# Performance work log

Measured on AMD Instinct MI355X. Metric: run time of the kernel, lower is better.

## Reference

```python
import math
import jax, jax.numpy as jnp
import numpy as np

B, T, D, NH = 4, 2048, 1024, 16
HS = D // NH
N_BUCKETS = 32
MAX_DIST = 128


def _relative_position_bucket(rp):
    # bidirectional T5 bucketing, n_buckets=32, max_distance=128
    nb = N_BUCKETS // 2  # 16
    buckets = (rp > 0).astype(jnp.int32) * nb
    rp = jnp.abs(rp)
    max_exact = nb // 2  # 8
    is_small = rp < max_exact
    me = max_exact - 1   # 7
    nbm = nb - 1         # 15
    rp_safe = jnp.maximum(rp, 1).astype(jnp.float32)
    rp_large = me + (jnp.log(rp_safe / me) / math.log(MAX_DIST / me) * (nbm - me)).astype(jnp.int32)
    rp_large = jnp.minimum(rp_large, nbm)
    buckets = buckets + jnp.where(is_small, rp, rp_large)
    return buckets


def compute_bias(rel_emb, qT, kT):
    ctx = jnp.arange(qT, dtype=jnp.int32)[:, None]
    mem = jnp.arange(kT, dtype=jnp.int32)[None, :]
    bucket = _relative_position_bucket(mem - ctx)  # [qT, kT]
    values = rel_emb[bucket]                        # [qT, kT, NH]
    return jnp.transpose(values, (2, 0, 1))[None]   # [1, NH, qT, kT]


def setup_inputs() -> dict:
    key = jax.random.key(0)
    ks = jax.random.split(key, 6)
    s = 0.02
    return {
        "queries": jax.random.normal(ks[0], (B, T, D), jnp.float32),
        "Wq": jax.random.normal(ks[1], (D, D), jnp.float32) * s,
        "Wk": jax.random.normal(ks[2], (D, D), jnp.float32) * s,
        "Wv": jax.random.normal(ks[3], (D, D), jnp.float32) * s,
        "Wo": jax.random.normal(ks[4], (D, D), jnp.float32) * s,
        "rel_emb": jax.random.normal(ks[5], (N_BUCKETS, NH), jnp.float32) * s,
    }


def reference(queries, Wq, Wk, Wv, Wo, rel_emb):
    b, t, d = queries.shape
    def split_heads(x):
        return jnp.transpose(x.reshape(b, t, NH, HS), (0, 2, 1, 3))  # [B, nh, T, hs]
    q = split_heads(queries @ Wq.T)
    k = split_heads(queries @ Wk.T)
    v = split_heads(queries @ Wv.T)
    att = jnp.einsum('bhqd,bhkd->bhqk', q, k) * (1.0 / math.sqrt(HS))
    att = att + compute_bias(rel_emb, t, t)
    att = jax.nn.softmax(att, axis=-1)
    o = jnp.einsum('bhqk,bhkd->bhqd', att, v)
    o = jnp.transpose(o, (0, 2, 1, 3)).reshape(b, t, d)
    return o @ Wo.T
```

## Files before the change

kernel.cpp:

```cpp
#include <hip/hip_runtime.h>
#include <math.h>

#define T_SEQ 2048
#define D_MODEL 1024
#define NHEADS 16
#define HSZ 64
#define BATCH 4

typedef __bf16 bf16x8 __attribute__((ext_vector_type(8)));
typedef __bf16 bf16x4 __attribute__((ext_vector_type(4)));
typedef short short4v __attribute__((ext_vector_type(4)));
typedef float f32x4 __attribute__((ext_vector_type(4)));
typedef float f32x16 __attribute__((ext_vector_type(16)));

__device__ __forceinline__ unsigned short f2bf(float f) {
    unsigned int u = __builtin_bit_cast(unsigned int, f);
    u += 0x7fff + ((u >> 16) & 1);
    return (unsigned short)(u >> 16);
}

__device__ __forceinline__ unsigned int pk2bf(float a, float b) {
#if __has_builtin(__builtin_amdgcn_cvt_pk_bf16_f32)
    typedef __bf16 bf16x2_t __attribute__((ext_vector_type(2)));
    bf16x2_t v = __builtin_amdgcn_cvt_pk_bf16_f32(a, b);
    return __builtin_bit_cast(unsigned int, v);
#else
    return (unsigned int)f2bf(a) | ((unsigned int)f2bf(b) << 16);
#endif
}

__device__ __forceinline__ float fexp2(float x) {
#if __has_builtin(__builtin_amdgcn_exp2f)
    return __builtin_amdgcn_exp2f(x);
#else
    return __builtin_exp2f(x);
#endif
}

__device__ __forceinline__ void gld_lds16(const void* g, void* lds) {
    __builtin_amdgcn_global_load_lds(
        (const __attribute__((address_space(1))) unsigned int*)g,
        (__attribute__((address_space(3))) unsigned int*)lds, 16, 0, 0);
}

__device__ __forceinline__ bf16x8 ld8(const unsigned short* p) {
    return *(const bf16x8*)p;
}

__device__ __forceinline__ float t5_bias(int delta, int h, const float* __restrict__ rel) {
    int bucket = delta > 0 ? 16 : 0;
    int arp = delta < 0 ? -delta : delta;
    if (arp < 8) {
        bucket += arp;
    } else {
        float f = logf((float)arp / 7.0f) * (8.0f / logf(128.0f / 7.0f));
        int rl = 7 + (int)f;
        bucket += rl < 15 ? rl : 15;
    }
    return rel[bucket * NHEADS + h] * 1.4426950408889634f;
}

__global__ void prep(const float* __restrict__ x,
                     const float* __restrict__ w0, const float* __restrict__ w1,
                     const float* __restrict__ w2, const float* __restrict__ w3,
                     unsigned short* __restrict__ Xbf,
                     unsigned short* __restrict__ Wbf) {
    int bid = blockIdx.x;
    int tid = threadIdx.x;
    if (bid < 8192) {
        int i = bid * 256 + tid;
        float4 v = ((const float4*)x)[i];
        ushort4 o;
        o.x = f2bf(v.x); o.y = f2bf(v.y); o.z = f2bf(v.z); o.w = f2bf(v.w);
        ((ushort4*)Xbf)[i] = o;
    } else {
        int wsel = (bid - 8192) >> 10;
        const float* srcs[4] = {w0, w1, w2, w3};
        int i = ((bid - 8192) & 1023) * 256 + tid;
        float4 v = ((const float4*)srcs[wsel])[i];
        ushort4 o;
        o.x = f2bf(v.x); o.y = f2bf(v.y); o.z = f2bf(v.z); o.w = f2bf(v.w);
        ((ushort4*)(Wbf + (size_t)wsel * 1048576))[i] = o;
    }
}

template<int MODE>
__global__ __launch_bounds__(256, 3) void gemm_bt(
    const unsigned short* __restrict__ A,
    const unsigned short* __restrict__ Bw,
    void* __restrict__ out)
{
    constexpr int K = 1024;
    __shared__ __align__(16) char smem[36864];
    unsigned short* As = (unsigned short*)smem;
    unsigned short* Bs = (unsigned short*)(smem + 16384);

    const int tid  = threadIdx.x;
    const int wave = tid >> 6;
    const int lane = tid & 63;
    const int quad = lane >> 4;
    const int l16  = lane & 15;
    const int wm   = wave >> 1;
    const int wn   = wave & 1;
    const int bn   = blockIdx.x;
    const int bm   = blockIdx.y;

    const int r_in = lane >> 3;
    const int lc   = (lane & 7) ^ r_in;

    f32x4 acc[4][4];
    #pragma unroll
    for (int m = 0; m < 4; ++m)
        #pragma unroll
        for (int n = 0; n < 4; ++n)
            acc[m][n] = f32x4{0.f, 0.f, 0.f, 0.f};

    const long a_row0 = (long)bm * 128;
    const long b_row0 = (long)bn * 128;

    for (int kt = 0; kt < K / 64; ++kt) {
        __syncthreads();
        const int k0 = kt * 64 + lc * 8;
        #pragma unroll
        for (int c = 0; c < 4; ++c) {
            int cc = wave * 4 + c;
            int r  = cc * 8 + r_in;
            gld_lds16(A  + (a_row0 + r) * K + k0, &As[cc * 512]);
            gld_lds16(Bw + (b_row0 + r) * K + k0, &Bs[cc * 512]);
        }
        __syncthreads();

        bf16x8 af[4][2], bf[4][2];
        #pragma unroll
        for (int m = 0; m < 4; ++m)
            #pragma unroll
            for (int ks = 0; ks < 2; ++ks) {
                int r  = wm * 64 + m * 16 + l16;
                int pc = (ks * 4 + quad) ^ (r & 7);
                af[m][ks] = ld8(&As[r * 64 + pc * 8]);
            }
        #pragma unroll
        for (int n = 0; n < 4; ++n)
            #pragma unroll
            for (int ks = 0; ks < 2; ++ks) {
                int r  = wn * 64 + n * 16 + l16;
                int pc = (ks * 4 + quad) ^ (r & 7);
                bf[n][ks] = ld8(&Bs[r * 64 + pc * 8]);
            }
        #pragma unroll
        for (int ks = 0; ks < 2; ++ks)
            #pragma unroll
            for (int m = 0; m < 4; ++m)
                #pragma unroll
                for (int n = 0; n < 4; ++n)
                    acc[m][n] = __builtin_amdgcn_mfma_f32_16x16x32_bf16(
                        af[m][ks], bf[n][ks], acc[m][n], 0, 0, 0);
    }

    const int which = (MODE == 4) ? (bn >> 3) : 0;
    if (MODE == 3) {
        float* O = (float*)out;
        #pragma unroll
        for (int m = 0; m < 4; ++m) {
            int row = bm * 128 + wm * 64 + m * 16 + quad * 4;
            #pragma unroll
            for (int n = 0; n < 4; ++n) {
                int col = bn * 128 + wn * 64 + n * 16 + l16;
                #pragma unroll
                for (int r = 0; r < 4; ++r)
                    O[(long)(row + r) * 1024 + col] = acc[m][n][r];
            }
        }
    } else if (which == 2) {
        unsigned short* O = (unsigned short*)out + (size_t)2 * 8388608;
        #pragma unroll
        for (int m = 0; m < 4; ++m) {
            int row = bm * 128 + wm * 64 + m * 16 + quad * 4;
            int b = row >> 11, t = row & 2047;
            #pragma unroll
            for (int n = 0; n < 4; ++n) {
                int cl = (bn * 128 + wn * 64 + n * 16 + l16) & 1023;
                int h = cl >> 6, hs = cl & 63;
                ushort4 pk;
                pk.x = f2bf(acc[m][n][0]); pk.y = f2bf(acc[m][n][1]);
                pk.z = f2bf(acc[m][n][2]); pk.w = f2bf(acc[m][n][3]);
                *(ushort4*)&O[(long)((b * 16 + h) * 64 + hs) * 2048 + t] = pk;
            }
        }
    } else {
        __syncthreads();
        unsigned short* Ew = (unsigned short*)smem + wave * 4608;
        const float qs = (which == 0) ? 0.125f * 1.4426950408889634f : 1.0f;
        #pragma unroll
        for (int m = 0; m < 4; ++m)
            #pragma unroll
            for (int n = 0; n < 4; ++n)
                #pragma unroll
                for (int r = 0; r < 4; ++r)
                    Ew[(m * 16 + quad * 4 + r) * 72 + n * 16 + l16] =
                        f2bf(acc[m][n][r] * qs);
        asm volatile("s_waitcnt lgkmcnt(0)" ::: "memory");

        const int cl0 = (bn * 128 + wn * 64) & 1023;
        const int h   = cl0 >> 6;
        const int gr0 = bm * 128 + wm * 64;
        const int b   = gr0 >> 11, t0 = gr0 & 2047;
        unsigned short* O = (unsigned short*)out + (size_t)which * 8388608
                          + ((size_t)(b * 16 + h) * 2048 + t0) * 64;
        #pragma unroll
        for (int rr = 0; rr < 8; ++rr) {
            int row   = rr * 8 + (lane >> 3);
            int chunk = lane & 7;
            uint4 v = *(const uint4*)&Ew[row * 72 + chunk * 8];
            *(uint4*)&O[(size_t)row * 64 + chunk * 8] = v;
        }
    }
}

__global__ __launch_bounds__(256, 3) void attn(
    const unsigned short* __restrict__ Q,
    const unsigned short* __restrict__ Kb,
    const unsigned short* __restrict__ Vt,
    const float* __restrict__ rel,
    unsigned short* __restrict__ AO)
{
    __shared__ __align__(16) char smem[33824];
    unsigned short* KsB = (unsigned short*)smem;
    unsigned short* VsB = (unsigned short*)(smem + 16384);
    float*          Bb  = (float*)(smem + 32768);

    const int tid  = threadIdx.x;
    const int wave = tid >> 6;
    const int lane = tid & 63;
    const int l31  = lane & 31;
    const int h5   = lane >> 5;

    const int bh = blockIdx.y;
    const int b  = bh >> 4, h = bh & 15;
    const int q0 = blockIdx.x * 128;

    const unsigned short* Qg = Q  + (long)bh * T_SEQ * HSZ;
    const unsigned short* Kg = Kb + (long)bh * T_SEQ * HSZ;
    const unsigned short* Vg = Vt + (long)bh * HSZ * T_SEQ;

    const int r_in = lane >> 3;
    const int lc   = (lane & 7) ^ r_in;

    {
        #pragma unroll
        for (int c = 0; c < 2; ++c) {
            int cc = wave * 2 + c;
            int r  = cc * 8 + r_in;
            gld_lds16(Kg + (long)r * 64 + lc * 8, &KsB[cc * 512]);
            gld_lds16(Vg + (long)r * T_SEQ + lc * 8, &VsB[cc * 512]);
        }
    }

    for (int i = tid; i < 263; i += 256)
        Bb[i] = t5_bias(i - 131, h, rel);

    const int qrow_lane = q0 + wave * 32 + l31;
    bf16x8 qf[4];
    #pragma unroll
    for (int hsc = 0; hsc < 4; ++hsc)
        qf[hsc] = ld8(&Qg[(long)qrow_lane * 64 + hsc * 16 + h5 * 8]);

    f32x16 o0 = {0.f,0.f,0.f,0.f,0.f,0.f,0.f,0.f,0.f,0.f,0.f,0.f,0.f,0.f,0.f,0.f};
    f32x16 o1 = o0;
    float li = 0.0f;

    const float cneg = rel[15 * NHEADS + h] * 1.4426950408889634f;
    const float cpos = rel[31 * NHEADS + h] * 1.4426950408889634f;

    for (int kt = 0; kt < T_SEQ / 64; ++kt) {
        const int cur = kt & 1;
        __syncthreads();

        if (kt + 1 < T_SEQ / 64) {
            unsigned short* Kn = KsB + (cur ^ 1) * 4096;
            unsigned short* Vn = VsB + (cur ^ 1) * 4096;
            #pragma unroll
            for (int c = 0; c < 2; ++c) {
                int cc = wave * 2 + c;
                int r  = cc * 8 + r_in;
                gld_lds16(Kg + (long)((kt + 1) * 64 + r) * 64 + lc * 8, &Kn[cc * 512]);
                gld_lds16(Vg + (long)r * T_SEQ + (kt + 1) * 64 + lc * 8, &Vn[cc * 512]);
            }
        }

        const unsigned short* Ks = KsB + cur * 4096;
        const unsigned short* Vs = VsB + cur * 4096;

        const int lo = kt * 64 - q0 - 127;
        const int hi = kt * 64 + 63 - q0;
        const bool outband = (lo >= 128) || (hi <= -128);
        const float cb = (lo >= 128) ? cpos : cneg;

        #pragma unroll
        for (int tt = 0; tt < 2; ++tt) {
            const int rk = tt * 32 + l31;
            bf16x8 af[4];
            #pragma unroll
            for (int hsc = 0; hsc < 4; ++hsc)
                af[hsc] = ld8(&Ks[rk * 64 + (((hsc << 1) | h5) ^ (rk & 7)) * 8]);

            f32x16 s;
            if (outband) {
                #pragma unroll
                for (int e = 0; e < 16; ++e) s[e] = cb;
            } else {
                const int ibase = kt * 64 + tt * 32 + h5 * 4 + 131 - qrow_lane;
                #pragma unroll
                for (int g = 0; g < 4; ++g) {
                    int i0 = ibase + g * 8;
                    i0 = i0 < 0 ? 0 : (i0 > 259 ? 259 : i0);
                    #pragma unroll
                    for (int r = 0; r < 4; ++r) s[g * 4 + r] = Bb[i0 + r];
                }
            }

            __builtin_amdgcn_s_setprio(1);
            #pragma unroll
            for (int hsc = 0; hsc < 4; ++hsc)
                s = __builtin_amdgcn_mfma_f32_32x32x16_bf16(af[hsc], qf[hsc], s, 0, 0, 0);
            __builtin_amdgcn_s_setprio(0);

            float p[16];
            #pragma unroll
            for (int e = 0; e < 16; ++e) p[e] = fexp2(s[e]);
            #pragma unroll
            for (int e = 0; e < 16; ++e) li += p[e];

            unsigned int x0 = pk2bf(p[0],  p[1]),  x1 = pk2bf(p[2],  p[3]);
            unsigned int y0 = pk2bf(p[4],  p[5]),  y1 = pk2bf(p[6],  p[7]);
            unsigned int z0 = pk2bf(p[8],  p[9]),  z1 = pk2bf(p[10], p[11]);
            unsigned int u0 = pk2bf(p[12], p[13]), u1 = pk2bf(p[14], p[15]);
            unsigned int sx0 = __shfl_xor((int)x0, 32), sx1 = __shfl_xor((int)x1, 32);
            unsigned int sy0 = __shfl_xor((int)y0, 32), sy1 = __shfl_xor((int)y1, 32);
            unsigned int sz0 = __shfl_xor((int)z0, 32), sz1 = __shfl_xor((int)z1, 32);
            unsigned int su0 = __shfl_xor((int)u0, 32), su1 = __shfl_xor((int)u1, 32);
            uint4 pw0, pw1;
            pw0.x = h5 ? sy0 : x0;  pw0.y = h5 ? sy1 : x1;
            pw0.z = h5 ? y0 : sx0;  pw0.w = h5 ? y1 : sx1;
            pw1.x = h5 ? su0 : z0;  pw1.y = h5 ? su1 : z1;
            pw1.z = h5 ? u0 : sz0;  pw1.w = h5 ? u1 : sz1;
            bf16x8 pf[2] = {__builtin_bit_cast(bf16x8, pw0),
                            __builtin_bit_cast(bf16x8, pw1)};

            #pragma unroll
            for (int c = 0; c < 2; ++c) {
                const int tc = tt * 2 + c;
                const int rv0 = l31;
                const int rv1 = 32 + l31;
                bf16x8 vf0 = ld8(&Vs[rv0 * 64 + (((tc << 1) | h5) ^ (rv0 & 7)) * 8]);
                bf16x8 vf1 = ld8(&Vs[rv1 * 64 + (((tc << 1) | h5) ^ (rv1 & 7)) * 8]);
                __builtin_amdgcn_s_setprio(1);
                o0 = __builtin_amdgcn_mfma_f32_32x32x16_bf16(pf[c], vf0, o0, 0, 0, 0);
                o1 = __builtin_amdgcn_mfma_f32_32x32x16_bf16(pf[c], vf1, o1, 0, 0, 0);
                __builtin_amdgcn_s_setprio(0);
            }
        }
    }

    li += __shfl_xor(li, 32);
    const float inv = 1.0f / li;

    #pragma unroll
    for (int g = 0; g < 4; ++g) {
        #pragma unroll
        for (int r = 0; r < 4; ++r) {
            const int ql = g * 8 + h5 * 4 + r;
            const float iv = __shfl(inv, ql);
            const int qrow = q0 + wave * 32 + ql;
            unsigned short* dst =
                &AO[(long)(b * T_SEQ + qrow) * D_MODEL + h * 64 + l31];
            dst[0]  = f2bf(o0[g * 4 + r] * iv);
            dst[32] = f2bf(o1[g * 4 + r] * iv);
        }
    }
}

extern "C" void kernel_launch(void* const* d_in, const int* in_sizes, int n_in,
                              void* d_out, int out_size, void* d_ws, size_t ws_size,
                              hipStream_t stream) {
    const float* x   = (const float*)d_in[0];
    const float* wq  = (const float*)d_in[1];
    const float* wk  = (const float*)d_in[2];
    const float* wv  = (const float*)d_in[3];
    const float* wo  = (const float*)d_in[4];
    const float* rel = (const float*)d_in[5];

    char* ws = (char*)d_ws;
    unsigned short* Xbf = (unsigned short*)(ws);
    unsigned short* Wbf = (unsigned short*)(ws + (16l << 20));
    unsigned short* Qb  = (unsigned short*)(ws + (24l << 20));

    prep<<<12288, 256, 0, stream>>>(x, wq, wk, wv, wo, Xbf, Wbf);

    gemm_bt<4><<<dim3(24, 64), 256, 0, stream>>>(Xbf, Wbf, Qb);

    unsigned short* Kbf = Qb + 8388608;
    unsigned short* Vtb = Qb + 16777216;
    unsigned short* AO  = Xbf;
    attn<<<dim3(16, 64), 256, 0, stream>>>(Qb, Kbf, Vtb, rel, AO);

    gemm_bt<3><<<dim3(8, 64), 256, 0, stream>>>(AO, Wbf + 3 * 1048576, d_out);
}
```

Baseline: 302.6 us.

## Use permlane32_swap for P shuffle, tree-sum li, retune launch bounds

Replaces the eight cross-half shfl_xor operations plus selects in the attention P-fragment build with four permlane32_swap intrinsics (with a shuffle fallback). It also reassociates the row-sum of exponentials into a tree. Launch bounds change to 2 blocks/CU for the GEMM and 4 for attention. Fewer LDS-based shuffles cut latency in the softmax-to-PV path, but raising attention occupancy to 4 may force register spills.

```diff
diff --git a/kernel.cpp b/kernel.cpp
--- a/kernel.cpp
+++ b/kernel.cpp
@@ -34,6 +34,21 @@
     return __builtin_amdgcn_exp2f(x);
 #else
     return __builtin_exp2f(x);
+#endif
+}
+
+__device__ __forceinline__ void pl32swap(unsigned int& a, unsigned int& b) {
+#if __has_builtin(__builtin_amdgcn_permlane32_swap)
+    auto r = __builtin_amdgcn_permlane32_swap((int)a, (int)b, false, false);
+    a = (unsigned int)r[0];
+    b = (unsigned int)r[1];
+#else
+    unsigned int sa = (unsigned int)__shfl_xor((int)a, 32);
+    unsigned int sb = (unsigned int)__shfl_xor((int)b, 32);
+    const int hi = (int)((threadIdx.x & 63) >> 5);
+    unsigned int na = hi ? sb : a;
+    unsigned int nb = hi ? b : sa;
+    a = na; b = nb;
 #endif
 }
 
@@ -85,7 +100,7 @@
 }
 
 template<int MODE>
-__global__ __launch_bounds__(256, 3) void gemm_bt(
+__global__ __launch_bounds__(256, 2) void gemm_bt(
     const unsigned short* __restrict__ A,
     const unsigned short* __restrict__ Bw,
     void* __restrict__ out)
@@ -217,7 +232,7 @@
     }
 }
 
-__global__ __launch_bounds__(256, 3) void attn(
+__global__ __launch_bounds__(256, 4) void attn(
     const unsigned short* __restrict__ Q,
     const unsigned short* __restrict__ Kb,
     const unsigned short* __restrict__ Vt,
@@ -328,22 +343,22 @@
             float p[16];
             #pragma unroll
             for (int e = 0; e < 16; ++e) p[e] = fexp2(s[e]);
-            #pragma unroll
-            for (int e = 0; e < 16; ++e) li += p[e];
+            {
+                float t0 = (p[0]  + p[1])  + (p[2]  + p[3]);
+                float t1 = (p[4]  + p[5])  + (p[6]  + p[7]);
+                float t2 = (p[8]  + p[9])  + (p[10] + p[11]);
+                float t3 = (p[12] + p[13]) + (p[14] + p[15]);
+                li += (t0 + t1) + (t2 + t3);
+            }
 
             unsigned int x0 = pk2bf(p[0],  p[1]),  x1 = pk2bf(p[2],  p[3]);
             unsigned int y0 = pk2bf(p[4],  p[5]),  y1 = pk2bf(p[6],  p[7]);
             unsigned int z0 = pk2bf(p[8],  p[9]),  z1 = pk2bf(p[10], p[11]);
             unsigned int u0 = pk2bf(p[12], p[13]), u1 = pk2bf(p[14], p[15]);
-            unsigned int sx0 = __shfl_xor((int)x0, 32), sx1 = __shfl_xor((int)x1, 32);
-            unsigned int sy0 = __shfl_xor((int)y0, 32), sy1 = __shfl_xor((int)y1, 32);
-            unsigned int sz0 = __shfl_xor((int)z0, 32), sz1 = __shfl_xor((int)z1, 32);
-            unsigned int su0 = __shfl_xor((int)u0, 32), su1 = __shfl_xor((int)u1, 32);
-            uint4 pw0, pw1;
-            pw0.x = h5 ? sy0 : x0;  pw0.y = h5 ? sy1 : x1;
-            pw0.z = h5 ? y0 : sx0;  pw0.w = h5 ? y1 : sx1;
-            pw1.x = h5 ? su0 : z0;  pw1.y = h5 ? su1 : z1;
-            pw1.z = h5 ? u0 : sz0;  pw1.w = h5 ? u1 : sz1;
+            pl32swap(x0, y0); pl32swap(x1, y1);
+            pl32swap(z0, u0); pl32swap(z1, u1);
+            uint4 pw0 = {x0, x1, y0, y1};
+            uint4 pw1 = {z0, z1, u0, u1};
             bf16x8 pf[2] = {__builtin_bit_cast(bf16x8, pw0),
                             __builtin_bit_cast(bf16x8, pw1)};
 
```

New measurement: 283.6 us. -6.3%, faster.
